# Kernel optimization log

Hardware: AMD Instinct MI355X
Metric: run time of the kernel (lower is better)

Reference implementation:

```python
import jax, jax.numpy as jnp
import numpy as np


def _conv1d(x, kernel, bias):
    # Keras Conv1D, padding='valid', stride 1. x: (b, ts, c); kernel: (K, c, f)
    y = jax.lax.conv_general_dilated(x, kernel, (1,), 'VALID',
                                     dimension_numbers=('NWC', 'WIO', 'NWC'))
    return y + bias


def setup_inputs() -> dict:
    key = jax.random.key(0)
    k1, k2, k3 = jax.random.split(key, 3)
    KSIZE, C, F = 5, 32, 32
    x = jax.random.normal(k1, (16, 65536, C), jnp.float32)
    Wconv = jax.random.normal(k2, (KSIZE, C, F), jnp.float32) * 0.05
    bconv = jnp.zeros((F,), jnp.float32)
    Wdef = jax.random.normal(k3, (KSIZE, 1), jnp.float32) * 0.1
    return {"x": x, "Wconv": Wconv, "bconv": bconv, "Wdef": Wdef}


def reference(x, Wconv, bconv, Wdef):
    K = Wconv.shape[0]
    # regularGrid: R = [-floor(K/2), ..., K-1-floor(K/2)]
    R = jnp.arange(K, dtype=jnp.float32) - (K // 2)
    offset = _conv1d(x, Wconv, bconv)                 # (b, ts-K+1, f)
    # dpn = mean over all positions of (offset + R) -> mean(offset) + R, shape (K,)
    pn = jnp.mean(offset) + R
    # g(Q, Q+pn) = max(0, 1 - |Q - (Q+pn)|) = max(0, 1 - |pn|): constant per tap
    scale = jnp.maximum(0.0, 1.0 - jnp.abs(pn))       # (K,)
    # y_k = scale_k * flatten(x); sum_k W_k * y_k == x * sum_k(W_k * scale_k)
    s = jnp.sum(Wdef[:, 0] * scale)                   # scalar
    y = x * s                                         # (b, ts, c)
    return _conv1d(y, Wconv, bconv)                   # (b, ts-K+1, f)
```

## Files before the change

### kernel.cpp

```cpp
#include <hip/hip_runtime.h>
#include <hip/hip_fp16.h>

#define T    65536
#define TOUT 65532
#define NB   16
#define CH   32
#define NF   32
#define KS   5
#define BM   128
#define NCHB 2048

typedef _Float16 f16x8 __attribute__((ext_vector_type(8)));
typedef _Float16 f16x4 __attribute__((ext_vector_type(4)));
typedef float    f32x4 __attribute__((ext_vector_type(4)));
typedef float    f32x4v __attribute__((ext_vector_type(4)));


__device__ __forceinline__ f16x4 cvt4v(f32x4v v) {
    f16x4 h;
    h[0] = (_Float16)v[0]; h[1] = (_Float16)v[1];
    h[2] = (_Float16)v[2]; h[3] = (_Float16)v[3];
    return h;
}
__device__ __forceinline__ f16x4 cvt4(float4 v) {
    f16x4 h;
    h[0] = (_Float16)v.x; h[1] = (_Float16)v.y;
    h[2] = (_Float16)v.z; h[3] = (_Float16)v.w;
    return h;
}

__global__ __launch_bounds__(256) void chsum4_kernel(const float* __restrict__ x,
                                                     _Float16* __restrict__ xh,
                                                     float* __restrict__ partials) {
    __shared__ float tot[CH];
    const int tid  = threadIdx.x;
    const int lane = tid & 63;
    if (tid < CH) tot[tid] = 0.f;
    __syncthreads();

    const f32x4v* x4  = (const f32x4v*)x;
    f16x4*        xh4 = (f16x4*)xh;
    const size_t idx4 = (size_t)blockIdx.x * 256 + tid;
    float s0 = 0.f, s1 = 0.f, s2 = 0.f, s3 = 0.f;
#pragma unroll
    for (int q = 0; q < 16; ++q) {
        size_t i = idx4 + (size_t)q * (NCHB * 256);
        f32x4v v = __builtin_nontemporal_load(&x4[i]);
        s0 += v[0]; s1 += v[1]; s2 += v[2]; s3 += v[3];
        xh4[i] = cvt4v(v);
    }
#pragma unroll
    for (int m = 8; m <= 32; m <<= 1) {
        s0 += __shfl_xor(s0, m, 64);
        s1 += __shfl_xor(s1, m, 64);
        s2 += __shfl_xor(s2, m, 64);
        s3 += __shfl_xor(s3, m, 64);
    }
    if (lane < 8) {
        const int c0 = lane * 4;
        atomicAdd(&tot[c0 + 0], s0);
        atomicAdd(&tot[c0 + 1], s1);
        atomicAdd(&tot[c0 + 2], s2);
        atomicAdd(&tot[c0 + 3], s3);
    }
    __syncthreads();
    if (tid < CH) partials[(size_t)blockIdx.x * CH + tid] = tot[tid];
}

__global__ __launch_bounds__(256) void scalar2_kernel(const float* __restrict__ x,
                                                      const float* __restrict__ Wconv,
                                                      const float* __restrict__ bconv,
                                                      const float* __restrict__ Wdef,
                                                      const float* __restrict__ partials,
                                                      float* __restrict__ ws) {
    __shared__ float ltot[CH];
    __shared__ float hb[4][CH], tb[4][CH];
    __shared__ float partial[256];
    const int tid = threadIdx.x;
    if (tid < CH) ltot[tid] = 0.f;
    __syncthreads();
    {
        const float4* p4 = (const float4*)partials;
        float s0 = 0.f, s1 = 0.f, s2 = 0.f, s3 = 0.f;
#pragma unroll 8
        for (int i = 0; i < 64; ++i) {
            float4 v = p4[i * 256 + tid];
            s0 += v.x; s1 += v.y; s2 += v.z; s3 += v.w;
        }
        int c0 = (tid & 7) * 4;
        atomicAdd(&ltot[c0 + 0], s0);
        atomicAdd(&ltot[c0 + 1], s1);
        atomicAdd(&ltot[c0 + 2], s2);
        atomicAdd(&ltot[c0 + 3], s3);
    }
    {
        int j = tid >> 5, c = tid & 31;
        int row = (j < 4) ? j : (T - 8 + j);
        float e = 0.f;
        for (int bb = 0; bb < NB; ++bb)
            e += x[((size_t)bb * T + row) * CH + c];
        if (j < 4) hb[j][c] = e; else tb[j - 4][c] = e;
    }
    __syncthreads();

    float term = 0.f;
    if (tid < KS * CH) {
        int k = tid >> 5, c = tid & 31;
        float wf = 0.f;
        const float* wp = &Wconv[(size_t)tid * NF];
        for (int f = 0; f < NF; ++f) wf += wp[f];
        float S = ltot[c];
        for (int jj = 0; jj < k; ++jj) S -= hb[jj][c];
        for (int jj = k; jj < 4; ++jj) S -= tb[jj][c];
        term = wf * S;
    }
    partial[tid] = term;
    __syncthreads();
    for (int off = 128; off > 0; off >>= 1) {
        if (tid < off) partial[tid] += partial[tid + off];
        __syncthreads();
    }
    if (tid == 0) {
        float sum_b = 0.f;
        for (int f = 0; f < NF; ++f) sum_b += bconv[f];
        float mean_off = partial[0] / (float)((size_t)NB * TOUT * NF) + sum_b / (float)NF;
        float s = 0.f;
        for (int k = 0; k < KS; ++k) {
            float pn = mean_off + (float)(k - 2);
            s += Wdef[k] * fmaxf(0.f, 1.f - fabsf(pn));
        }
        ws[CH] = s;
    }
}

__global__ __launch_bounds__(256) void conv2_kernel(const _Float16* __restrict__ xh,
                                                    const float* __restrict__ Wconv,
                                                    const float* __restrict__ bconv,
                                                    const float* __restrict__ ws,
                                                    float* __restrict__ out) {
    __shared__ _Float16 A[(BM + 4) * 40];
    __shared__ _Float16 Wt[KS * CH * 40];

    const int tid = threadIdx.x;
    const int b   = blockIdx.y;
    const int t0  = blockIdx.x * BM;
    const int c0  = (tid & 7) * 4;

    {
        const f16x4* xh4 = (const f16x4*)xh;
        for (int r = (tid >> 3); r < BM + 4; r += 32) {
            int t = t0 + r;
            f16x4 h = {};
            if (t < T) h = xh4[((size_t)b * T + t) * 8 + (tid & 7)];
            *(f16x4*)&A[r * 40 + c0] = h;
        }
    }
    {
        const float4* w4 = (const float4*)Wconv;
#pragma unroll
        for (int j = 0; j < 5; ++j) {
            int i4 = tid + j * 256;
            float4 v = w4[i4];
            int fi = i4 * 4;
            int k = fi >> 10, c = (fi >> 5) & 31, f = fi & 31;
            _Float16* wrow = &Wt[(k * CH + f) * 40 + c];
            wrow[0 * 40] = (_Float16)v.x;
            wrow[1 * 40] = (_Float16)v.y;
            wrow[2 * 40] = (_Float16)v.z;
            wrow[3 * 40] = (_Float16)v.w;
        }
    }
    __syncthreads();

    const int lane = tid & 63;
    const int wave = tid >> 6;
    const int rowbase = wave * 32;
    const int lrow = lane & 15;
    const int kgrp = lane >> 4;

    f32x4 acc00 = {}, acc01 = {}, acc10 = {}, acc11 = {};
#pragma unroll
    for (int kk = 0; kk < KS; ++kk) {
        f16x8 a0 = *(const f16x8*)&A[(rowbase + lrow + kk) * 40 + kgrp * 8];
        f16x8 a1 = *(const f16x8*)&A[(rowbase + 16 + lrow + kk) * 40 + kgrp * 8];
        f16x8 b0 = *(const f16x8*)&Wt[(kk * CH + lrow) * 40 + kgrp * 8];
        f16x8 b1 = *(const f16x8*)&Wt[(kk * CH + 16 + lrow) * 40 + kgrp * 8];
        acc00 = __builtin_amdgcn_mfma_f32_16x16x32_f16(a0, b0, acc00, 0, 0, 0);
        acc01 = __builtin_amdgcn_mfma_f32_16x16x32_f16(a0, b1, acc01, 0, 0, 0);
        acc10 = __builtin_amdgcn_mfma_f32_16x16x32_f16(a1, b0, acc10, 0, 0, 0);
        acc11 = __builtin_amdgcn_mfma_f32_16x16x32_f16(a1, b1, acc11, 0, 0, 0);
    }

    float sv  = ws[CH];
    int col0  = lane & 15;
    float bc0 = bconv[col0], bc1 = bconv[col0 + 16];
    int rbase = rowbase + ((lane >> 4) << 2);
#pragma unroll
    for (int reg = 0; reg < 4; ++reg) {
        int t = t0 + rbase + reg;
        if (t < TOUT) {
            float* o = &out[((size_t)b * TOUT + t) * NF];
            o[col0]      = sv * acc00[reg] + bc0;
            o[col0 + 16] = sv * acc01[reg] + bc1;
        }
        int t1 = t + 16;
        if (t1 < TOUT) {
            float* o = &out[((size_t)b * TOUT + t1) * NF];
            o[col0]      = sv * acc10[reg] + bc0;
            o[col0 + 16] = sv * acc11[reg] + bc1;
        }
    }
}

__global__ __launch_bounds__(256) void chsum3_kernel(const float* __restrict__ x,
                                                     float* __restrict__ partials) {
    __shared__ float tot[CH];
    const int tid = threadIdx.x;
    if (tid < CH) tot[tid] = 0.f;
    __syncthreads();
    const float4* x4 = (const float4*)x;
    const size_t idx4 = (size_t)blockIdx.x * 256 + tid;
    float s0 = 0.f, s1 = 0.f, s2 = 0.f, s3 = 0.f;
#pragma unroll
    for (int q = 0; q < 16; ++q) {
        float4 v = x4[idx4 + (size_t)q * (NCHB * 256)];
        s0 += v.x; s1 += v.y; s2 += v.z; s3 += v.w;
    }
    const int c0 = (tid & 7) * 4;
    atomicAdd(&tot[c0 + 0], s0);
    atomicAdd(&tot[c0 + 1], s1);
    atomicAdd(&tot[c0 + 2], s2);
    atomicAdd(&tot[c0 + 3], s3);
    __syncthreads();
    if (tid < CH) partials[(size_t)blockIdx.x * CH + tid] = tot[tid];
}

__global__ __launch_bounds__(256) void conv_kernel(const float* __restrict__ x,
                                                   const float* __restrict__ Wconv,
                                                   const float* __restrict__ bconv,
                                                   const float* __restrict__ ws,
                                                   float* __restrict__ out) {
    __shared__ _Float16 A[(BM + 4) * 40];
    __shared__ _Float16 Wt[KS * CH * 40];
    int tid = threadIdx.x;
    int b   = blockIdx.y;
    int t0  = blockIdx.x * BM;
    {
        int c0 = (tid & 7) * 4;
        for (int r = (tid >> 3); r < BM + 4; r += 32) {
            int t = t0 + r;
            float4 v = make_float4(0.f, 0.f, 0.f, 0.f);
            if (t < T) v = *(const float4*)&x[((size_t)b * T + t) * CH + c0];
            *(f16x4*)&A[r * 40 + c0] = cvt4(v);
        }
    }
    if (tid < KS * CH) {
        int k = tid >> 5, c = tid & 31;
        const float* wp = &Wconv[(size_t)tid * NF];
        for (int f = 0; f < NF; ++f)
            Wt[(k * CH + f) * 40 + c] = (_Float16)wp[f];
    }
    __syncthreads();
    int lane = tid & 63;
    int wave = tid >> 6;
    int rowbase = wave * 32;
    int lrow = lane & 15;
    int kgrp = lane >> 4;
    f32x4 acc00 = {}, acc01 = {}, acc10 = {}, acc11 = {};
#pragma unroll
    for (int kk = 0; kk < KS; ++kk) {
        f16x8 a0 = *(const f16x8*)&A[(rowbase + lrow + kk) * 40 + kgrp * 8];
        f16x8 a1 = *(const f16x8*)&A[(rowbase + 16 + lrow + kk) * 40 + kgrp * 8];
        f16x8 b0 = *(const f16x8*)&Wt[(kk * CH + lrow) * 40 + kgrp * 8];
        f16x8 b1 = *(const f16x8*)&Wt[(kk * CH + 16 + lrow) * 40 + kgrp * 8];
        acc00 = __builtin_amdgcn_mfma_f32_16x16x32_f16(a0, b0, acc00, 0, 0, 0);
        acc01 = __builtin_amdgcn_mfma_f32_16x16x32_f16(a0, b1, acc01, 0, 0, 0);
        acc10 = __builtin_amdgcn_mfma_f32_16x16x32_f16(a1, b0, acc10, 0, 0, 0);
        acc11 = __builtin_amdgcn_mfma_f32_16x16x32_f16(a1, b1, acc11, 0, 0, 0);
    }
    float sv  = ws[CH];
    int col0  = lane & 15;
    float bc0 = bconv[col0], bc1 = bconv[col0 + 16];
    int rbase = rowbase + ((lane >> 4) << 2);
#pragma unroll
    for (int reg = 0; reg < 4; ++reg) {
        int t = t0 + rbase + reg;
        if (t < TOUT) {
            float* o = &out[((size_t)b * TOUT + t) * NF];
            o[col0]      = sv * acc00[reg] + bc0;
            o[col0 + 16] = sv * acc01[reg] + bc1;
        }
        int t1 = t + 16;
        if (t1 < TOUT) {
            float* o = &out[((size_t)b * TOUT + t1) * NF];
            o[col0]      = sv * acc10[reg] + bc0;
            o[col0 + 16] = sv * acc11[reg] + bc1;
        }
    }
}

extern "C" void kernel_launch(void* const* d_in, const int* in_sizes, int n_in,
                              void* d_out, int out_size, void* d_ws, size_t ws_size,
                              hipStream_t stream) {
    const float* x     = (const float*)d_in[0];
    const float* Wconv = (const float*)d_in[1];
    const float* bconv = (const float*)d_in[2];
    const float* Wdef  = (const float*)d_in[3];
    float* out      = (float*)d_out;
    float* ws       = (float*)d_ws;
    float* partials = ws + 64;
    _Float16* xh    = (_Float16*)((char*)d_ws + 524288);

    const size_t need = 524288 + (size_t)NB * T * CH * sizeof(_Float16);
    dim3 grid((TOUT + BM - 1) / BM, NB);

    if (ws_size >= need) {
        chsum4_kernel<<<dim3(NCHB), dim3(256), 0, stream>>>(x, xh, partials);
        scalar2_kernel<<<dim3(1), dim3(256), 0, stream>>>(x, Wconv, bconv, Wdef, partials, ws);
        conv2_kernel<<<grid, dim3(256), 0, stream>>>(xh, Wconv, bconv, ws, out);
    } else {
        chsum3_kernel<<<dim3(NCHB), dim3(256), 0, stream>>>(x, partials);
        scalar2_kernel<<<dim3(1), dim3(256), 0, stream>>>(x, Wconv, bconv, Wdef, partials, ws);
        conv_kernel<<<grid, dim3(256), 0, stream>>>(x, Wconv, bconv, ws, out);
    }
}
```

Baseline: 86.56 us.

## Fuse channel-sum, scalar and conv into one persistent kernel with grid barrier

Replaces the three-kernel pipeline (sum plus fp16 copy, scalar reduction, conv) with a single persistent kernel of 1024 co-resident blocks. Each block sums its own 1024-row slice, publishes a partial, then waits at a global atomic-counter barrier. Every block then recomputes the scalar redundantly and runs the MFMA conv over its slice, with the next tile's loads overlapped with the current tile's MFMA work. This drops the fp16 intermediate write and read and two launch gaps. In exchange x is read twice, the barrier depends on all blocks being resident (checked via an occupancy query), and a memset is added.

```diff
diff --git a/kernel.cpp b/kernel.cpp
--- a/kernel.cpp
+++ b/kernel.cpp
@@ -1,14 +1,16 @@
 #include <hip/hip_runtime.h>
 #include <hip/hip_fp16.h>
 
-#define T    65536
-#define TOUT 65532
-#define NB   16
-#define CH   32
-#define NF   32
-#define KS   5
-#define BM   128
-#define NCHB 2048
+#define T     65536
+#define TOUT  65532
+#define NB    16
+#define CH    32
+#define NF    32
+#define KS    5
+#define BM    128
+#define RPB   1024
+#define NBLKM 1024
+#define NCHB  2048
 
 typedef _Float16 f16x8 __attribute__((ext_vector_type(8)));
 typedef _Float16 f16x4 __attribute__((ext_vector_type(4)));
@@ -16,17 +18,219 @@
 typedef float    f32x4v __attribute__((ext_vector_type(4)));
 
 
+__device__ __forceinline__ f16x4 cvt4(float4 v) {
+    f16x4 h;
+    h[0] = (_Float16)v.x; h[1] = (_Float16)v.y;
+    h[2] = (_Float16)v.z; h[3] = (_Float16)v.w;
+    return h;
+}
 __device__ __forceinline__ f16x4 cvt4v(f32x4v v) {
     f16x4 h;
     h[0] = (_Float16)v[0]; h[1] = (_Float16)v[1];
     h[2] = (_Float16)v[2]; h[3] = (_Float16)v[3];
     return h;
 }
-__device__ __forceinline__ f16x4 cvt4(float4 v) {
-    f16x4 h;
-    h[0] = (_Float16)v.x; h[1] = (_Float16)v.y;
-    h[2] = (_Float16)v.z; h[3] = (_Float16)v.w;
-    return h;
+
+__global__ __launch_bounds__(256, 4) void mono3_kernel(
+    const float* __restrict__ x, const float* __restrict__ Wconv,
+    const float* __restrict__ bconv, const float* __restrict__ Wdef,
+    float* __restrict__ ws, float* __restrict__ out)
+{
+    __shared__ _Float16 A[(BM + 4) * 40];
+    __shared__ _Float16 Wt[KS * CH * 40];
+    __shared__ float ltot[CH];
+    __shared__ float hb[4][CH], tb[4][CH];
+    __shared__ float partial[256];
+    __shared__ float s_sh;
+
+    const int tid  = threadIdx.x;
+    const int lane = tid & 63;
+    const int bid  = blockIdx.x;
+    const int b    = bid >> 6;
+    const int tb0  = (bid & 63) * RPB;
+    const int c0   = (tid & 7) * 4;
+    const float* xb = x + (size_t)b * T * CH;
+    float* partials = ws + 64;
+    unsigned int* cnt = (unsigned int*)ws + 40;
+
+    {
+        const float4* w4 = (const float4*)Wconv;
+#pragma unroll
+        for (int j = 0; j < 5; ++j) {
+            int i4 = tid + j * 256;
+            float4 v = w4[i4];
+            int fi = i4 * 4;
+            int k = fi >> 10, c = (fi >> 5) & 31, f = fi & 31;
+            _Float16* wrow = &Wt[(k * CH + f) * 40 + c];
+            wrow[0 * 40] = (_Float16)v.x;
+            wrow[1 * 40] = (_Float16)v.y;
+            wrow[2 * 40] = (_Float16)v.z;
+            wrow[3 * 40] = (_Float16)v.w;
+        }
+    }
+    if (tid < CH) ltot[tid] = 0.f;
+    __syncthreads();
+
+    {
+        const float4* xr = (const float4*)(xb + (size_t)tb0 * CH);
+        float s0 = 0.f, s1 = 0.f, s2 = 0.f, s3 = 0.f;
+#pragma unroll 8
+        for (int q = 0; q < 32; ++q) {
+            float4 v = xr[q * 256 + tid];
+            s0 += v.x; s1 += v.y; s2 += v.z; s3 += v.w;
+        }
+#pragma unroll
+        for (int m = 8; m <= 32; m <<= 1) {
+            s0 += __shfl_xor(s0, m, 64);
+            s1 += __shfl_xor(s1, m, 64);
+            s2 += __shfl_xor(s2, m, 64);
+            s3 += __shfl_xor(s3, m, 64);
+        }
+        if (lane < 8) {
+            const int cc = lane * 4;
+            atomicAdd(&ltot[cc + 0], s0);
+            atomicAdd(&ltot[cc + 1], s1);
+            atomicAdd(&ltot[cc + 2], s2);
+            atomicAdd(&ltot[cc + 3], s3);
+        }
+    }
+    __syncthreads();
+    if (tid < CH)
+        __hip_atomic_store(&partials[(size_t)bid * CH + tid], ltot[tid],
+                           __ATOMIC_RELEASE, __HIP_MEMORY_SCOPE_AGENT);
+
+    float4 rv0, rv1, rv2, rv3, rvh;
+    const int srow = tid >> 3;
+    auto LOADJ = [&](int j) {
+        const float* p = xb + (size_t)(tb0 + j * BM + srow) * CH + c0;
+        rv0 = *(const float4*)(p);
+        rv1 = *(const float4*)(p + 32 * CH);
+        rv2 = *(const float4*)(p + 64 * CH);
+        rv3 = *(const float4*)(p + 96 * CH);
+        if (tid < 32) {
+            int t = tb0 + j * BM + 128 + srow;
+            rvh = (t < T) ? *(const float4*)(xb + (size_t)t * CH + c0)
+                          : make_float4(0.f, 0.f, 0.f, 0.f);
+        }
+    };
+    auto WRITEJ = [&]() {
+        *(f16x4*)&A[(srow     ) * 40 + c0] = cvt4(rv0);
+        *(f16x4*)&A[(srow + 32) * 40 + c0] = cvt4(rv1);
+        *(f16x4*)&A[(srow + 64) * 40 + c0] = cvt4(rv2);
+        *(f16x4*)&A[(srow + 96) * 40 + c0] = cvt4(rv3);
+        if (tid < 32)
+            *(f16x4*)&A[(128 + srow) * 40 + c0] = cvt4(rvh);
+    };
+    LOADJ(0);
+
+    __syncthreads();
+    if (tid == 0) {
+        __hip_atomic_fetch_add(cnt, 1u, __ATOMIC_ACQ_REL, __HIP_MEMORY_SCOPE_AGENT);
+        unsigned int guard = 0;
+        while (__hip_atomic_load(cnt, __ATOMIC_ACQUIRE, __HIP_MEMORY_SCOPE_AGENT)
+                   < (unsigned)NBLKM) {
+            __builtin_amdgcn_s_sleep(8);
+            if (++guard > (1u << 27)) break;
+        }
+    }
+    __syncthreads();
+
+    if (tid < CH) ltot[tid] = 0.f;
+    __syncthreads();
+    {
+        float acc = 0.f;
+#pragma unroll 16
+        for (int q = 0; q < 128; ++q)
+            acc += __hip_atomic_load(&partials[q * 256 + tid],
+                                     __ATOMIC_RELAXED, __HIP_MEMORY_SCOPE_AGENT);
+        atomicAdd(&ltot[tid & 31], acc);
+    }
+    {
+        int j = tid >> 5, c = tid & 31;
+        int row = (j < 4) ? j : (T - 8 + j);
+        float e = 0.f;
+        for (int bb = 0; bb < NB; ++bb)
+            e += x[((size_t)bb * T + row) * CH + c];
+        if (j < 4) hb[j][c] = e; else tb[j - 4][c] = e;
+    }
+    __syncthreads();
+
+    float term = 0.f;
+    if (tid < KS * CH) {
+        int k = tid >> 5, c = tid & 31;
+        float wf = 0.f;
+        const float* wp = &Wconv[(size_t)tid * NF];
+        for (int f = 0; f < NF; ++f) wf += wp[f];
+        float S = ltot[c];
+        for (int jj = 0; jj < k; ++jj) S -= hb[jj][c];
+        for (int jj = k; jj < 4; ++jj) S -= tb[jj][c];
+        term = wf * S;
+    }
+    partial[tid] = term;
+    __syncthreads();
+    for (int off = 128; off > 0; off >>= 1) {
+        if (tid < off) partial[tid] += partial[tid + off];
+        __syncthreads();
+    }
+    if (tid == 0) {
+        float sum_b = 0.f;
+        for (int f = 0; f < NF; ++f) sum_b += bconv[f];
+        float mean_off = partial[0] / (float)((size_t)NB * TOUT * NF) + sum_b / (float)NF;
+        float sv = 0.f;
+        for (int k = 0; k < KS; ++k) {
+            float pn = mean_off + (float)(k - 2);
+            sv += Wdef[k] * fmaxf(0.f, 1.f - fabsf(pn));
+        }
+        s_sh = sv;
+    }
+    __syncthreads();
+
+    const int wave    = tid >> 6;
+    const int rowbase = wave * 32;
+    const int lrow    = lane & 15;
+    const int kgrp    = lane >> 4;
+    const int col0    = lane & 15;
+    const float sv    = s_sh;
+    const float bc0   = bconv[col0], bc1 = bconv[col0 + 16];
+
+#pragma unroll
+    for (int j = 0; j < 8; ++j) {
+        __syncthreads();
+        WRITEJ();
+        if (j < 7) LOADJ(j + 1);
+        __syncthreads();
+
+        f32x4 acc00 = {}, acc01 = {}, acc10 = {}, acc11 = {};
+#pragma unroll
+        for (int kk = 0; kk < KS; ++kk) {
+            f16x8 a0 = *(const f16x8*)&A[(rowbase + lrow + kk) * 40 + kgrp * 8];
+            f16x8 a1 = *(const f16x8*)&A[(rowbase + 16 + lrow + kk) * 40 + kgrp * 8];
+            f16x8 b0 = *(const f16x8*)&Wt[(kk * CH + lrow) * 40 + kgrp * 8];
+            f16x8 b1 = *(const f16x8*)&Wt[(kk * CH + 16 + lrow) * 40 + kgrp * 8];
+            acc00 = __builtin_amdgcn_mfma_f32_16x16x32_f16(a0, b0, acc00, 0, 0, 0);
+            acc01 = __builtin_amdgcn_mfma_f32_16x16x32_f16(a0, b1, acc01, 0, 0, 0);
+            acc10 = __builtin_amdgcn_mfma_f32_16x16x32_f16(a1, b0, acc10, 0, 0, 0);
+            acc11 = __builtin_amdgcn_mfma_f32_16x16x32_f16(a1, b1, acc11, 0, 0, 0);
+        }
+
+        int tsub  = tb0 + j * BM;
+        int rbase = rowbase + ((lane >> 4) << 2);
+#pragma unroll
+        for (int reg = 0; reg < 4; ++reg) {
+            int t = tsub + rbase + reg;
+            if (t < TOUT) {
+                float* o = &out[((size_t)b * TOUT + t) * NF];
+                o[col0]      = sv * acc00[reg] + bc0;
+                o[col0 + 16] = sv * acc01[reg] + bc1;
+            }
+            int t1 = t + 16;
+            if (t1 < TOUT) {
+                float* o = &out[((size_t)b * TOUT + t1) * NF];
+                o[col0]      = sv * acc10[reg] + bc0;
+                o[col0 + 16] = sv * acc11[reg] + bc1;
+            }
+        }
+    }
 }
 
 __global__ __launch_bounds__(256) void chsum4_kernel(const float* __restrict__ x,
@@ -37,7 +241,6 @@
     const int lane = tid & 63;
     if (tid < CH) tot[tid] = 0.f;
     __syncthreads();
-
     const f32x4v* x4  = (const f32x4v*)x;
     f16x4*        xh4 = (f16x4*)xh;
     const size_t idx4 = (size_t)blockIdx.x * 256 + tid;
@@ -57,11 +260,11 @@
         s3 += __shfl_xor(s3, m, 64);
     }
     if (lane < 8) {
-        const int c0 = lane * 4;
-        atomicAdd(&tot[c0 + 0], s0);
-        atomicAdd(&tot[c0 + 1], s1);
-        atomicAdd(&tot[c0 + 2], s2);
-        atomicAdd(&tot[c0 + 3], s3);
+        const int cc = lane * 4;
+        atomicAdd(&tot[cc + 0], s0);
+        atomicAdd(&tot[cc + 1], s1);
+        atomicAdd(&tot[cc + 2], s2);
+        atomicAdd(&tot[cc + 3], s3);
     }
     __syncthreads();
     if (tid < CH) partials[(size_t)blockIdx.x * CH + tid] = tot[tid];
@@ -87,11 +290,11 @@
             float4 v = p4[i * 256 + tid];
             s0 += v.x; s1 += v.y; s2 += v.z; s3 += v.w;
         }
-        int c0 = (tid & 7) * 4;
-        atomicAdd(&ltot[c0 + 0], s0);
-        atomicAdd(&ltot[c0 + 1], s1);
-        atomicAdd(&ltot[c0 + 2], s2);
-        atomicAdd(&ltot[c0 + 3], s3);
+        int cc = (tid & 7) * 4;
+        atomicAdd(&ltot[cc + 0], s0);
+        atomicAdd(&ltot[cc + 1], s1);
+        atomicAdd(&ltot[cc + 2], s2);
+        atomicAdd(&ltot[cc + 3], s3);
     }
     {
         int j = tid >> 5, c = tid & 31;
@@ -102,7 +305,6 @@
         if (j < 4) hb[j][c] = e; else tb[j - 4][c] = e;
     }
     __syncthreads();
-
     float term = 0.f;
     if (tid < KS * CH) {
         int k = tid >> 5, c = tid & 31;
@@ -140,12 +342,10 @@
                                                     float* __restrict__ out) {
     __shared__ _Float16 A[(BM + 4) * 40];
     __shared__ _Float16 Wt[KS * CH * 40];
-
     const int tid = threadIdx.x;
     const int b   = blockIdx.y;
     const int t0  = blockIdx.x * BM;
     const int c0  = (tid & 7) * 4;
-
     {
         const f16x4* xh4 = (const f16x4*)xh;
         for (int r = (tid >> 3); r < BM + 4; r += 32) {
@@ -171,101 +371,11 @@
         }
     }
     __syncthreads();
-
     const int lane = tid & 63;
     const int wave = tid >> 6;
     const int rowbase = wave * 32;
     const int lrow = lane & 15;
     const int kgrp = lane >> 4;
-
-    f32x4 acc00 = {}, acc01 = {}, acc10 = {}, acc11 = {};
-#pragma unroll
-    for (int kk = 0; kk < KS; ++kk) {
-        f16x8 a0 = *(const f16x8*)&A[(rowbase + lrow + kk) * 40 + kgrp * 8];
-        f16x8 a1 = *(const f16x8*)&A[(rowbase + 16 + lrow + kk) * 40 + kgrp * 8];
-        f16x8 b0 = *(const f16x8*)&Wt[(kk * CH + lrow) * 40 + kgrp * 8];
-        f16x8 b1 = *(const f16x8*)&Wt[(kk * CH + 16 + lrow) * 40 + kgrp * 8];
-        acc00 = __builtin_amdgcn_mfma_f32_16x16x32_f16(a0, b0, acc00, 0, 0, 0);
-        acc01 = __builtin_amdgcn_mfma_f32_16x16x32_f16(a0, b1, acc01, 0, 0, 0);
-        acc10 = __builtin_amdgcn_mfma_f32_16x16x32_f16(a1, b0, acc10, 0, 0, 0);
-        acc11 = __builtin_amdgcn_mfma_f32_16x16x32_f16(a1, b1, acc11, 0, 0, 0);
-    }
-
-    float sv  = ws[CH];
-    int col0  = lane & 15;
-    float bc0 = bconv[col0], bc1 = bconv[col0 + 16];
-    int rbase = rowbase + ((lane >> 4) << 2);
-#pragma unroll
-    for (int reg = 0; reg < 4; ++reg) {
-        int t = t0 + rbase + reg;
-        if (t < TOUT) {
-            float* o = &out[((size_t)b * TOUT + t) * NF];
-            o[col0]      = sv * acc00[reg] + bc0;
-            o[col0 + 16] = sv * acc01[reg] + bc1;
-        }
-        int t1 = t + 16;
-        if (t1 < TOUT) {
-            float* o = &out[((size_t)b * TOUT + t1) * NF];
-            o[col0]      = sv * acc10[reg] + bc0;
-            o[col0 + 16] = sv * acc11[reg] + bc1;
-        }
-    }
-}
-
-__global__ __launch_bounds__(256) void chsum3_kernel(const float* __restrict__ x,
-                                                     float* __restrict__ partials) {
-    __shared__ float tot[CH];
-    const int tid = threadIdx.x;
-    if (tid < CH) tot[tid] = 0.f;
-    __syncthreads();
-    const float4* x4 = (const float4*)x;
-    const size_t idx4 = (size_t)blockIdx.x * 256 + tid;
-    float s0 = 0.f, s1 = 0.f, s2 = 0.f, s3 = 0.f;
-#pragma unroll
-    for (int q = 0; q < 16; ++q) {
-        float4 v = x4[idx4 + (size_t)q * (NCHB * 256)];
-        s0 += v.x; s1 += v.y; s2 += v.z; s3 += v.w;
-    }
-    const int c0 = (tid & 7) * 4;
-    atomicAdd(&tot[c0 + 0], s0);
-    atomicAdd(&tot[c0 + 1], s1);
-    atomicAdd(&tot[c0 + 2], s2);
-    atomicAdd(&tot[c0 + 3], s3);
-    __syncthreads();
-    if (tid < CH) partials[(size_t)blockIdx.x * CH + tid] = tot[tid];
-}
-
-__global__ __launch_bounds__(256) void conv_kernel(const float* __restrict__ x,
-                                                   const float* __restrict__ Wconv,
-                                                   const float* __restrict__ bconv,
-                                                   const float* __restrict__ ws,
-                                                   float* __restrict__ out) {
-    __shared__ _Float16 A[(BM + 4) * 40];
-    __shared__ _Float16 Wt[KS * CH * 40];
-    int tid = threadIdx.x;
-    int b   = blockIdx.y;
-    int t0  = blockIdx.x * BM;
-    {
-        int c0 = (tid & 7) * 4;
-        for (int r = (tid >> 3); r < BM + 4; r += 32) {
-            int t = t0 + r;
-            float4 v = make_float4(0.f, 0.f, 0.f, 0.f);
-            if (t < T) v = *(const float4*)&x[((size_t)b * T + t) * CH + c0];
-            *(f16x4*)&A[r * 40 + c0] = cvt4(v);
-        }
-    }
-    if (tid < KS * CH) {
-        int k = tid >> 5, c = tid & 31;
-        const float* wp = &Wconv[(size_t)tid * NF];
-        for (int f = 0; f < NF; ++f)
-            Wt[(k * CH + f) * 40 + c] = (_Float16)wp[f];
-    }
-    __syncthreads();
-    int lane = tid & 63;
-    int wave = tid >> 6;
-    int rowbase = wave * 32;
-    int lrow = lane & 15;
-    int kgrp = lane >> 4;
     f32x4 acc00 = {}, acc01 = {}, acc10 = {}, acc11 = {};
 #pragma unroll
     for (int kk = 0; kk < KS; ++kk) {
@@ -311,16 +421,19 @@
     float* partials = ws + 64;
     _Float16* xh    = (_Float16*)((char*)d_ws + 524288);
 
-    const size_t need = 524288 + (size_t)NB * T * CH * sizeof(_Float16);
-    dim3 grid((TOUT + BM - 1) / BM, NB);
-
-    if (ws_size >= need) {
+    hipMemsetAsync(ws, 0, 256, stream);
+
+    int nb = 0;
+    (void)hipOccupancyMaxActiveBlocksPerMultiprocessor(&nb, mono3_kernel, 256, 0);
+
+    if (nb >= 4 && ws_size >= 524288) {
+        mono3_kernel<<<dim3(NBLKM), dim3(256), 0, stream>>>(x, Wconv, bconv, Wdef, ws, out);
+    } else {
+        const size_t need = 524288 + (size_t)NB * T * CH * sizeof(_Float16);
+        dim3 grid((TOUT + BM - 1) / BM, NB);
         chsum4_kernel<<<dim3(NCHB), dim3(256), 0, stream>>>(x, xh, partials);
         scalar2_kernel<<<dim3(1), dim3(256), 0, stream>>>(x, Wconv, bconv, Wdef, partials, ws);
         conv2_kernel<<<grid, dim3(256), 0, stream>>>(xh, Wconv, bconv, ws, out);
-    } else {
-        chsum3_kernel<<<dim3(NCHB), dim3(256), 0, stream>>>(x, partials);
-        scalar2_kernel<<<dim3(1), dim3(256), 0, stream>>>(x, Wconv, bconv, Wdef, partials, ws);
-        conv_kernel<<<grid, dim3(256), 0, stream>>>(x, Wconv, bconv, ws, out);
-    }
-}
+        (void)need;
+    }
+}
```

Result: slower. 91.44 us (+5.6%).
